# Kernel optimization log

Measured on AMD Instinct MI355X. Metric: run time of the kernel, lower is better.

Reference implementation:

```python
import jax, jax.numpy as jnp
import numpy as np

N = 100000   # amino-acid nodes
D = 128      # prot_hidden_dim == input_dim (output_dim)
E = 600000   # edges per relation
L = 3        # prot_num_layers
EPS = 1e-5   # BatchNorm eps


def setup_inputs() -> dict:
    key = jax.random.key(0)
    ks = jax.random.split(key, 16)
    x = jax.random.normal(ks[0], (N, D), jnp.float32)
    seq_src = jax.random.randint(ks[1], (E,), 0, N)
    seq_dst = jax.random.randint(ks[2], (E,), 0, N)
    knn_src = jax.random.randint(ks[3], (E,), 0, N)
    knn_dst = jax.random.randint(ks[4], (E,), 0, N)
    dis_src = jax.random.randint(ks[5], (E,), 0, N)
    dis_dst = jax.random.randint(ks[6], (E,), 0, N)
    # GraphConv weights/biases: [layer, relation, ...]
    Wrel = jax.random.normal(ks[7], (L, 3, D, D), jnp.float32) * (1.0 / np.sqrt(D))
    brel = jax.random.normal(ks[8], (L, 3, D), jnp.float32) * 0.02
    # per-layer fc (last maps hidden -> output_dim == D)
    Wfc = jax.random.normal(ks[9], (L, D, D), jnp.float32) * (1.0 / np.sqrt(D))
    bfc = jax.random.normal(ks[10], (L, D), jnp.float32) * 0.02
    # BatchNorm (eval mode) for layers l=0,1
    gamma = 1.0 + 0.1 * jax.random.normal(ks[11], (L - 1, D), jnp.float32)
    beta = 0.1 * jax.random.normal(ks[12], (L - 1, D), jnp.float32)
    run_mean = 0.1 * jax.random.normal(ks[13], (L - 1, D), jnp.float32)
    run_var = jax.random.uniform(ks[14], (L - 1, D), jnp.float32, 0.5, 1.5)
    return dict(x=x, seq_src=seq_src, seq_dst=seq_dst, knn_src=knn_src,
                knn_dst=knn_dst, dis_src=dis_src, dis_dst=dis_dst,
                Wrel=Wrel, brel=brel, Wfc=Wfc, bfc=bfc,
                gamma=gamma, beta=beta, run_mean=run_mean, run_var=run_var)


def _deg_norms(src, dst):
    # DGL norm='both': out-degree of src, in-degree of dst, clamped to >=1
    ones = jnp.ones(src.shape, jnp.float32)
    out_deg = jnp.clip(jax.ops.segment_sum(ones, src, num_segments=N), 1.0)
    in_deg = jnp.clip(jax.ops.segment_sum(ones, dst, num_segments=N), 1.0)
    return out_deg ** -0.5, in_deg ** -0.5


def reference(x, seq_src, seq_dst, knn_src, knn_dst, dis_src, dis_dst,
              Wrel, brel, Wfc, bfc, gamma, beta, run_mean, run_var):
    rels = [(seq_src, seq_dst), (knn_src, knn_dst), (dis_src, dis_dst)]
    norms = [_deg_norms(s, d) for s, d in rels]
    h = x
    for l in range(L):
        agg = jnp.zeros((N, D), h.dtype)
        for r, (s, d) in enumerate(rels):
            ns, nd = norms[r]
            # GraphConv norm='both', in==out feats: weight first, then propagate
            m = (h @ Wrel[l, r]) * ns[:, None]           # [N, D]
            msg = jax.ops.segment_sum(m[s], d, num_segments=N)  # gather-scatter
            agg = agg + msg * nd[:, None] + brel[l, r]
        h = agg @ Wfc[l] + bfc[l]
        if l < L - 1:
            # eval-mode BatchNorm1d + ReLU (dropout is identity in eval)
            h = (h - run_mean[l]) * jax.lax.rsqrt(run_var[l] + EPS) * gamma[l] + beta[l]
            h = jax.nn.relu(h)
    return h
```

## Files before the change

kernel.cpp:

```cpp
#include <hip/hip_runtime.h>
#include <math.h>

#define N_NODES 100000
#define D 128
#define E_EDGES 600000
#define BN_EPS 1e-5f

typedef __attribute__((ext_vector_type(8))) __bf16 bf16x8;
typedef __attribute__((ext_vector_type(4))) __bf16 bf16x4;
typedef __attribute__((ext_vector_type(16))) float f32x16;

__device__ __forceinline__ int qswz(int row, int q) {
    return (q & 8) | ((q ^ row) & 7);
}
__device__ __forceinline__ int swz(int row, int c) { return c ^ ((row >> 1) & 3); }

__global__ __launch_bounds__(256) void hist_kernel(
    const int* __restrict__ s0, const int* __restrict__ d0,
    const int* __restrict__ s1, const int* __restrict__ d1,
    const int* __restrict__ s2, const int* __restrict__ d2,
    int* __restrict__ outdeg, int* __restrict__ indeg)
{
    const int r = blockIdx.y;
    const int* src = (r == 0) ? s0 : ((r == 1) ? s1 : s2);
    const int* dst = (r == 0) ? d0 : ((r == 1) ? d1 : d2);
    int* od = outdeg + (size_t)r * N_NODES;
    int* id = indeg + (size_t)r * N_NODES;
    int i4 = blockIdx.x * 256 + threadIdx.x;
    if (i4 < E_EDGES / 4) {
        int4 s = ((const int4*)src)[i4];
        int4 d = ((const int4*)dst)[i4];
        atomicAdd(&od[s.x], 1); atomicAdd(&od[s.y], 1);
        atomicAdd(&od[s.z], 1); atomicAdd(&od[s.w], 1);
        atomicAdd(&id[d.x], 1); atomicAdd(&id[d.y], 1);
        atomicAdd(&id[d.z], 1); atomicAdd(&id[d.w], 1);
    }
}

__global__ __launch_bounds__(256) void norm_kernel(
    const int* __restrict__ outdeg, const int* __restrict__ indeg,
    float* __restrict__ ns, float* __restrict__ nd)
{
    int n = blockIdx.x * 256 + threadIdx.x;
    int r = blockIdx.y;
    if (n < N_NODES) {
        int od = outdeg[r * N_NODES + n];
        int id = indeg[r * N_NODES + n];
        ns[r * N_NODES + n] = rsqrtf((float)(od < 1 ? 1 : od));
        nd[r * N_NODES + n] = rsqrtf((float)(id < 1 ? 1 : id));
    }
}

__global__ __launch_bounds__(1024) void scan_kernel(
    const int* __restrict__ indeg, int* __restrict__ rowptr, int* __restrict__ cursor)
{
    const int r = blockIdx.x;
    const int4* deg4 = (const int4*)(indeg + (size_t)r * N_NODES);
    int* rp = rowptr + (size_t)r * (N_NODES + 1);
    int* cur = cursor + (size_t)r * N_NODES;

    __shared__ int wsum[16];
    __shared__ int woff[16];
    __shared__ int chunk_total;

    const int tid = threadIdx.x;
    const int lane = tid & 63;
    const int wid = tid >> 6;
    const int N4 = N_NODES / 4;

    int running = 0;
    for (int base4 = 0; base4 < N4; base4 += 1024) {
        int i4 = base4 + tid;
        int4 v = (i4 < N4) ? deg4[i4] : make_int4(0, 0, 0, 0);
        int s0 = v.x, s1 = s0 + v.y, s2 = s1 + v.z, s3 = s2 + v.w;

        int x = s3;
        #pragma unroll
        for (int off = 1; off < 64; off <<= 1) {
            int y = __shfl_up(x, off);
            if (lane >= off) x += y;
        }
        if (lane == 63) wsum[wid] = x;
        __syncthreads();
        if (wid == 0) {
            int t = (lane < 16) ? wsum[lane] : 0;
            int xx = t;
            #pragma unroll
            for (int off = 1; off < 16; off <<= 1) {
                int y = __shfl_up(xx, off);
                if (lane >= off) xx += y;
            }
            if (lane < 16) woff[lane] = xx - t;
            if (lane == 15) chunk_total = xx;
        }
        __syncthreads();

        int texcl = x - s3;
        int offset = running + woff[wid] + texcl;
        if (i4 < N4) {
            int idx = i4 * 4;
            rp[idx]     = offset;       cur[idx]     = offset;
            rp[idx + 1] = offset + s0;  cur[idx + 1] = offset + s0;
            rp[idx + 2] = offset + s1;  cur[idx + 2] = offset + s1;
            rp[idx + 3] = offset + s2;  cur[idx + 3] = offset + s2;
        }
        running += chunk_total;
    }
    if (tid == 0) rp[N_NODES] = running;
}

__global__ __launch_bounds__(256) void fill_kernel(
    const int* __restrict__ s0, const int* __restrict__ d0,
    const int* __restrict__ s1, const int* __restrict__ d1,
    const int* __restrict__ s2, const int* __restrict__ d2,
    const float* __restrict__ nsv,
    int* __restrict__ cursor, int2* __restrict__ eint)
{
    const int r = blockIdx.y;
    const int* src = (r == 0) ? s0 : ((r == 1) ? s1 : s2);
    const int* dst = (r == 0) ? d0 : ((r == 1) ? d1 : d2);
    int* cur = cursor + (size_t)r * N_NODES;
    int2* eg = eint + (size_t)r * E_EDGES;
    const float* ns_ = nsv + (size_t)r * N_NODES;
    int i = blockIdx.x * 256 + threadIdx.x;
    if (i < E_EDGES) {
        int s = src[i];
        int d = dst[i];
        int pos = atomicAdd(&cur[d], 1);
        eg[pos] = make_int2(s, __float_as_int(ns_[s]));
    }
}

__global__ __launch_bounds__(256) void wprep_kernel(
    const float* __restrict__ Wrel, const float* __restrict__ Wfc,
    const float* __restrict__ gma, const float* __restrict__ rvar,
    __bf16* __restrict__ Whi, __bf16* __restrict__ Wlo)
{
    __shared__ float W1[128][132];
    __shared__ float W2[128][132];
    const int b = blockIdx.x;
    const int l = b / 3;
    const int t = threadIdx.x;

    const float* src1 = Wrel + (size_t)b * D * D;
    const float* src2 = Wfc + (size_t)l * D * D;
    #pragma unroll
    for (int p = 0; p < 16; ++p) {
        int u = t + p * 256;
        int r = u >> 5, f = u & 31;
        float4 v1 = *(const float4*)(src1 + r * D + f * 4);
        float4 v2 = *(const float4*)(src2 + r * D + f * 4);
        *(float4*)&W1[r][f * 4] = v1;
        *(float4*)&W2[r][f * 4] = v2;
    }
    __syncthreads();

    const int row = t >> 1;
    const int cb = (t & 1) * 64;
    float4 acc4[16];
    #pragma unroll
    for (int j = 0; j < 16; ++j) acc4[j] = make_float4(0.f, 0.f, 0.f, 0.f);
    for (int k = 0; k < 128; ++k) {
        float a = W1[row][k];
        #pragma unroll
        for (int j = 0; j < 16; ++j) {
            float4 w = *(const float4*)&W2[k][cb + j * 4];
            acc4[j].x = fmaf(a, w.x, acc4[j].x);
            acc4[j].y = fmaf(a, w.y, acc4[j].y);
            acc4[j].z = fmaf(a, w.z, acc4[j].z);
            acc4[j].w = fmaf(a, w.w, acc4[j].w);
        }
    }
    for (int j = 0; j < 64; ++j) {
        int colj = cb + j;
        float s = 1.0f;
        if (l < 2) s = gma[l * D + colj] * rsqrtf(rvar[l * D + colj] + BN_EPS);
        float v = (&acc4[j >> 2].x)[j & 3] * s;
        __bf16 h = (__bf16)v;
        __bf16 lo = (__bf16)(v - (float)h);
        Whi[((size_t)b * D + colj) * D + row] = h;
        Wlo[((size_t)b * D + colj) * D + row] = lo;
    }
}

__global__ __launch_bounds__(128) void bias_prep_kernel(
    const float* __restrict__ brel, const float* __restrict__ Wfc,
    const float* __restrict__ bfc,
    const float* __restrict__ gma, const float* __restrict__ bta,
    const float* __restrict__ rmean, const float* __restrict__ rvar,
    float* __restrict__ bvec)
{
    int j = threadIdx.x;
    int l = blockIdx.x;
    float acc = bfc[l * D + j];
    for (int k = 0; k < D; ++k) {
        float bs = brel[(l * 3 + 0) * D + k] + brel[(l * 3 + 1) * D + k] + brel[(l * 3 + 2) * D + k];
        acc = fmaf(bs, Wfc[((size_t)l * D + k) * D + j], acc);
    }
    if (l < 2) {
        float s = gma[l * D + j] * rsqrtf(rvar[l * D + j] + BN_EPS);
        acc = acc * s + (bta[l * D + j] - rmean[l * D + j] * s);
    }
    bvec[l * D + j] = acc;
}

__global__ __launch_bounds__(512, 6) void fused_layer_kernel(
    const float* __restrict__ h,
    const int* __restrict__ rowptr,
    const int2* __restrict__ eint,
    const float* __restrict__ ndv,
    const __bf16* __restrict__ Whi,
    const __bf16* __restrict__ Wlo,
    float* __restrict__ out, const float* __restrict__ bias, int relu)
{
    __shared__ __bf16 Ah[64 * 128];
    __shared__ __bf16 Al[64 * 128];
    __shared__ __bf16 Bh[128 * 32];
    __shared__ __bf16 Bl[128 * 32];

    const int t = threadIdx.x;
    const int lane = t & 63;
    const int wid = t >> 6;
    const int wrow = wid & 1;
    const int wcol = wid >> 1;
    const int row0 = blockIdx.x * 64;

    const int g = t >> 3;
    const int gl = t & 7;

    f32x16 acc;
    #pragma unroll
    for (int i = 0; i < 16; ++i) acc[i] = 0.0f;

    for (int r = 0; r < 3; ++r) {
        const int* rp = rowptr + (size_t)r * (N_NODES + 1);
        const int2* eg = eint + (size_t)r * E_EDGES;
        const float* nd_ = ndv + (size_t)r * N_NODES;

        {
            int rowl = g;
            int grow = row0 + rowl;
            float4 a0 = {0,0,0,0}, a1 = {0,0,0,0}, a2 = {0,0,0,0}, a3 = {0,0,0,0};
            if (grow < N_NODES) {
                int beg = rp[grow], end = rp[grow + 1];
                float sc = nd_[grow];
                int e = beg;
                for (; e + 1 < end; e += 2) {
                    int2 e0 = eg[e];
                    int2 e1 = eg[e + 1];
                    float w0 = __int_as_float(e0.y);
                    float w1 = __int_as_float(e1.y);
                    const float* hp0 = h + (size_t)e0.x * D + gl * 4;
                    const float* hp1 = h + (size_t)e1.x * D + gl * 4;
                    float4 u0 = *(const float4*)(hp0);
                    float4 u1 = *(const float4*)(hp0 + 32);
                    float4 u2 = *(const float4*)(hp0 + 64);
                    float4 u3 = *(const float4*)(hp0 + 96);
                    float4 v0 = *(const float4*)(hp1);
                    float4 v1 = *(const float4*)(hp1 + 32);
                    float4 v2 = *(const float4*)(hp1 + 64);
                    float4 v3 = *(const float4*)(hp1 + 96);
                    a0.x = fmaf(w0, u0.x, a0.x); a0.y = fmaf(w0, u0.y, a0.y);
                    a0.z = fmaf(w0, u0.z, a0.z); a0.w = fmaf(w0, u0.w, a0.w);
                    a1.x = fmaf(w0, u1.x, a1.x); a1.y = fmaf(w0, u1.y, a1.y);
                    a1.z = fmaf(w0, u1.z, a1.z); a1.w = fmaf(w0, u1.w, a1.w);
                    a2.x = fmaf(w0, u2.x, a2.x); a2.y = fmaf(w0, u2.y, a2.y);
                    a2.z = fmaf(w0, u2.z, a2.z); a2.w = fmaf(w0, u2.w, a2.w);
                    a3.x = fmaf(w0, u3.x, a3.x); a3.y = fmaf(w0, u3.y, a3.y);
                    a3.z = fmaf(w0, u3.z, a3.z); a3.w = fmaf(w0, u3.w, a3.w);
                    a0.x = fmaf(w1, v0.x, a0.x); a0.y = fmaf(w1, v0.y, a0.y);
                    a0.z = fmaf(w1, v0.z, a0.z); a0.w = fmaf(w1, v0.w, a0.w);
                    a1.x = fmaf(w1, v1.x, a1.x); a1.y = fmaf(w1, v1.y, a1.y);
                    a1.z = fmaf(w1, v1.z, a1.z); a1.w = fmaf(w1, v1.w, a1.w);
                    a2.x = fmaf(w1, v2.x, a2.x); a2.y = fmaf(w1, v2.y, a2.y);
                    a2.z = fmaf(w1, v2.z, a2.z); a2.w = fmaf(w1, v2.w, a2.w);
                    a3.x = fmaf(w1, v3.x, a3.x); a3.y = fmaf(w1, v3.y, a3.y);
                    a3.z = fmaf(w1, v3.z, a3.z); a3.w = fmaf(w1, v3.w, a3.w);
                }
                if (e < end) {
                    int2 e0 = eg[e];
                    float w0 = __int_as_float(e0.y);
                    const float* hp0 = h + (size_t)e0.x * D + gl * 4;
                    float4 u0 = *(const float4*)(hp0);
                    float4 u1 = *(const float4*)(hp0 + 32);
                    float4 u2 = *(const float4*)(hp0 + 64);
                    float4 u3 = *(const float4*)(hp0 + 96);
                    a0.x = fmaf(w0, u0.x, a0.x); a0.y = fmaf(w0, u0.y, a0.y);
                    a0.z = fmaf(w0, u0.z, a0.z); a0.w = fmaf(w0, u0.w, a0.w);
                    a1.x = fmaf(w0, u1.x, a1.x); a1.y = fmaf(w0, u1.y, a1.y);
                    a1.z = fmaf(w0, u1.z, a1.z); a1.w = fmaf(w0, u1.w, a1.w);
                    a2.x = fmaf(w0, u2.x, a2.x); a2.y = fmaf(w0, u2.y, a2.y);
                    a2.z = fmaf(w0, u2.z, a2.z); a2.w = fmaf(w0, u2.w, a2.w);
                    a3.x = fmaf(w0, u3.x, a3.x); a3.y = fmaf(w0, u3.y, a3.y);
                    a3.z = fmaf(w0, u3.z, a3.z); a3.w = fmaf(w0, u3.w, a3.w);
                }
                a0.x *= sc; a0.y *= sc; a0.z *= sc; a0.w *= sc;
                a1.x *= sc; a1.y *= sc; a1.z *= sc; a1.w *= sc;
                a2.x *= sc; a2.y *= sc; a2.z *= sc; a2.w *= sc;
                a3.x *= sc; a3.y *= sc; a3.z *= sc; a3.w *= sc;
            }
            float4 av[4] = {a0, a1, a2, a3};
            #pragma unroll
            for (int j = 0; j < 4; ++j) {
                int q = (gl >> 1) + 4 * j;
                int idx = rowl * 128 + qswz(rowl, q) * 8 + (gl & 1) * 4;
                bf16x4 hv, lv;
                float* ap = &av[j].x;
                #pragma unroll
                for (int c = 0; c < 4; ++c) {
                    __bf16 hb = (__bf16)ap[c];
                    hv[c] = hb;
                    lv[c] = (__bf16)(ap[c] - (float)hb);
                }
                *(bf16x4*)&Ah[idx] = hv;
                *(bf16x4*)&Al[idx] = lv;
            }
        }

        for (int ks = 0; ks < 4; ++ks) {
            {
                int colj = t >> 2;
                int c = t & 3;
                int idx = colj * 32 + swz(colj, c) * 8;
                const __bf16* sh = Whi + (size_t)r * D * D + (size_t)colj * D + ks * 32 + c * 8;
                const __bf16* sl = Wlo + (size_t)r * D * D + (size_t)colj * D + ks * 32 + c * 8;
                *(bf16x8*)&Bh[idx] = *(const bf16x8*)sh;
                *(bf16x8*)&Bl[idx] = *(const bf16x8*)sl;
            }
            __syncthreads();

            const int arow = lane & 31;
            const int kgrp = lane >> 5;
            #pragma unroll
            for (int ksub = 0; ksub < 2; ++ksub) {
                int ac = ksub * 2 + kgrp;
                int arow_g = wrow * 32 + arow;
                int q = ks * 4 + ac;
                int aidx = arow_g * 128 + qswz(arow_g, q) * 8;
                bf16x8 ahv = *(const bf16x8*)&Ah[aidx];
                bf16x8 alv = *(const bf16x8*)&Al[aidx];
                int colg = wcol * 32 + arow;
                int bidx = colg * 32 + swz(colg, ac) * 8;
                bf16x8 bhv = *(const bf16x8*)&Bh[bidx];
                bf16x8 blv = *(const bf16x8*)&Bl[bidx];
                acc = __builtin_amdgcn_mfma_f32_32x32x16_bf16(ahv, bhv, acc, 0, 0, 0);
                acc = __builtin_amdgcn_mfma_f32_32x32x16_bf16(ahv, blv, acc, 0, 0, 0);
                acc = __builtin_amdgcn_mfma_f32_32x32x16_bf16(alv, bhv, acc, 0, 0, 0);
            }
            __syncthreads();
        }
    }

    const int colb = lane & 31;
    const int rq = lane >> 5;
    {
        int colg = wcol * 32 + colb;
        float bv = bias[colg];
        #pragma unroll
        for (int reg = 0; reg < 16; ++reg) {
            int rowl = wrow * 32 + (reg & 3) + 8 * (reg >> 2) + 4 * rq;
            int grow = row0 + rowl;
            if (grow < N_NODES) {
                float z = acc[reg] + bv;
                if (relu) z = z > 0.f ? z : 0.f;
                out[(size_t)grow * D + colg] = z;
            }
        }
    }
}

extern "C" void kernel_launch(void* const* d_in, const int* in_sizes, int n_in,
                              void* d_out, int out_size, void* d_ws, size_t ws_size,
                              hipStream_t stream)
{
    const float* x      = (const float*)d_in[0];
    const int* seq_src  = (const int*)d_in[1];
    const int* seq_dst  = (const int*)d_in[2];
    const int* knn_src  = (const int*)d_in[3];
    const int* knn_dst  = (const int*)d_in[4];
    const int* dis_src  = (const int*)d_in[5];
    const int* dis_dst  = (const int*)d_in[6];
    const float* Wrel   = (const float*)d_in[7];
    const float* brel   = (const float*)d_in[8];
    const float* Wfc    = (const float*)d_in[9];
    const float* bfc    = (const float*)d_in[10];
    const float* gma    = (const float*)d_in[11];
    const float* bta    = (const float*)d_in[12];
    const float* rmean  = (const float*)d_in[13];
    const float* rvar   = (const float*)d_in[14];
    float* out = (float*)d_out;

    const size_t ND = (size_t)N_NODES * D;
    float* ws   = (float*)d_ws;
    float* h0   = ws;
    float* h1   = h0 + ND;
    float* ns_  = h1 + ND;
    float* nd_  = ns_ + 3 * N_NODES;
    float* bvec = nd_ + 3 * N_NODES;
    __bf16* Whi = (__bf16*)(bvec + 3 * D);
    __bf16* Wlo = Whi + (size_t)9 * D * D;
    int* outdeg = (int*)(Wlo + (size_t)9 * D * D);
    int* indeg  = outdeg + 3 * N_NODES;
    int* rowptr = indeg + 3 * N_NODES;
    int* cursor = rowptr + 3 * (N_NODES + 1) + 1;
    int2* eint  = (int2*)(cursor + 3 * N_NODES);

    hipMemsetAsync(outdeg, 0, (size_t)6 * N_NODES * sizeof(int), stream);
    hist_kernel<<<dim3((E_EDGES / 4 + 255) / 256, 3), 256, 0, stream>>>(
        seq_src, seq_dst, knn_src, knn_dst, dis_src, dis_dst, outdeg, indeg);
    norm_kernel<<<dim3((N_NODES + 255) / 256, 3), 256, 0, stream>>>(outdeg, indeg, ns_, nd_);
    scan_kernel<<<3, 1024, 0, stream>>>(indeg, rowptr, cursor);
    fill_kernel<<<dim3((E_EDGES + 255) / 256, 3), 256, 0, stream>>>(
        seq_src, seq_dst, knn_src, knn_dst, dis_src, dis_dst, ns_, cursor, eint);

    wprep_kernel<<<9, 256, 0, stream>>>(Wrel, Wfc, gma, rvar, Whi, Wlo);
    bias_prep_kernel<<<3, 128, 0, stream>>>(brel, Wfc, bfc, gma, bta, rmean, rvar, bvec);

    const int GB = (N_NODES + 63) / 64;
    fused_layer_kernel<<<GB, 512, 0, stream>>>(
        x, rowptr, eint, nd_, Whi, Wlo, h0, bvec, 1);
    fused_layer_kernel<<<GB, 512, 0, stream>>>(
        h0, rowptr, eint, nd_, Whi + (size_t)3 * D * D, Wlo + (size_t)3 * D * D,
        h1, bvec + D, 1);
    fused_layer_kernel<<<GB, 512, 0, stream>>>(
        h1, rowptr, eint, nd_, Whi + (size_t)6 * D * D, Wlo + (size_t)6 * D * D,
        out, bvec + 2 * D, 0);
}
```

Before: 946.0 us.

## Parallelize CSR scan and enlarge fused layer tiles to 128 rows

Replaces the three-block serial prefix scan with a three-kernel decoupled scan (per-block partial, mid carry, add), so building the CSR row pointers uses many blocks. The fused gather+MFMA layer kernel moves to 128-row tiles with 1024 threads: each 16-lane group gathers two rows with contiguous 8-float segments and 4-way edge unrolling, the LDS swizzle is simplified, and B staging is issued right after each k-step barrier instead of before it. Output stores become nontemporal. The larger block raises LDS use and register pressure and halves the number of blocks, which may reduce occupancy or load balance.

```diff
diff --git a/kernel.cpp b/kernel.cpp
--- a/kernel.cpp
+++ b/kernel.cpp
@@ -5,14 +5,15 @@
 #define D 128
 #define E_EDGES 600000
 #define BN_EPS 1e-5f
+#define RPS (N_NODES + 4)
+#define N4V (N_NODES / 4)
+#define SCAN_BLOCKS ((N4V + 255) / 256)
 
 typedef __attribute__((ext_vector_type(8))) __bf16 bf16x8;
 typedef __attribute__((ext_vector_type(4))) __bf16 bf16x4;
 typedef __attribute__((ext_vector_type(16))) float f32x16;
 
-__device__ __forceinline__ int qswz(int row, int q) {
-    return (q & 8) | ((q ^ row) & 7);
-}
+__device__ __forceinline__ int qswz(int row, int q) { return q ^ (row & 15); }
 __device__ __forceinline__ int swz(int row, int c) { return c ^ ((row >> 1) & 3); }
 
 __global__ __launch_bounds__(256) void hist_kernel(
@@ -51,62 +52,72 @@
     }
 }
 
-__global__ __launch_bounds__(1024) void scan_kernel(
-    const int* __restrict__ indeg, int* __restrict__ rowptr, int* __restrict__ cursor)
-{
-    const int r = blockIdx.x;
-    const int4* deg4 = (const int4*)(indeg + (size_t)r * N_NODES);
-    int* rp = rowptr + (size_t)r * (N_NODES + 1);
-    int* cur = cursor + (size_t)r * N_NODES;
-
-    __shared__ int wsum[16];
-    __shared__ int woff[16];
-    __shared__ int chunk_total;
-
-    const int tid = threadIdx.x;
-    const int lane = tid & 63;
-    const int wid = tid >> 6;
-    const int N4 = N_NODES / 4;
-
-    int running = 0;
-    for (int base4 = 0; base4 < N4; base4 += 1024) {
-        int i4 = base4 + tid;
-        int4 v = (i4 < N4) ? deg4[i4] : make_int4(0, 0, 0, 0);
-        int s0 = v.x, s1 = s0 + v.y, s2 = s1 + v.z, s3 = s2 + v.w;
-
-        int x = s3;
+__global__ __launch_bounds__(256) void scan_part_kernel(
+    const int* __restrict__ indeg, int* __restrict__ rowptr, int* __restrict__ bsum)
+{
+    const int r = blockIdx.y;
+    const int t = threadIdx.x;
+    const int lane = t & 63, wid = t >> 6;
+    __shared__ int wsum[4], woff[4];
+    int i4 = blockIdx.x * 256 + t;
+    int4 v = (i4 < N4V) ? ((const int4*)(indeg + (size_t)r * N_NODES))[i4]
+                        : make_int4(0, 0, 0, 0);
+    int s0 = v.x, s1 = s0 + v.y, s2 = s1 + v.z, s3 = s2 + v.w;
+    int x = s3;
+    #pragma unroll
+    for (int off = 1; off < 64; off <<= 1) {
+        int y = __shfl_up(x, off);
+        if (lane >= off) x += y;
+    }
+    if (lane == 63) wsum[wid] = x;
+    __syncthreads();
+    if (t < 4) { int s = 0; for (int j = 0; j < t; ++j) s += wsum[j]; woff[t] = s; }
+    __syncthreads();
+    int base = woff[wid] + (x - s3);
+    if (i4 < N4V) {
+        int idx = i4 * 4;
+        int* rp = rowptr + (size_t)r * RPS;
+        rp[idx] = base; rp[idx + 1] = base + s0; rp[idx + 2] = base + s1; rp[idx + 3] = base + s2;
+    }
+    if (t == 255) bsum[r * SCAN_BLOCKS + blockIdx.x] = woff[3] + wsum[3];
+}
+
+__global__ __launch_bounds__(256) void scan_mid_kernel(
+    int* __restrict__ bsum, int* __restrict__ rowptr)
+{
+    const int t = threadIdx.x;
+    const int lane = t & 63, wid = t >> 6;
+    if (wid >= 3) return;
+    const int r = wid;
+    int carry = 0;
+    for (int c = 0; c < (SCAN_BLOCKS + 63) / 64; ++c) {
+        int idx = c * 64 + lane;
+        int v = (idx < SCAN_BLOCKS) ? bsum[r * SCAN_BLOCKS + idx] : 0;
+        int x = v;
         #pragma unroll
         for (int off = 1; off < 64; off <<= 1) {
             int y = __shfl_up(x, off);
             if (lane >= off) x += y;
         }
-        if (lane == 63) wsum[wid] = x;
-        __syncthreads();
-        if (wid == 0) {
-            int t = (lane < 16) ? wsum[lane] : 0;
-            int xx = t;
-            #pragma unroll
-            for (int off = 1; off < 16; off <<= 1) {
-                int y = __shfl_up(xx, off);
-                if (lane >= off) xx += y;
-            }
-            if (lane < 16) woff[lane] = xx - t;
-            if (lane == 15) chunk_total = xx;
-        }
-        __syncthreads();
-
-        int texcl = x - s3;
-        int offset = running + woff[wid] + texcl;
-        if (i4 < N4) {
-            int idx = i4 * 4;
-            rp[idx]     = offset;       cur[idx]     = offset;
-            rp[idx + 1] = offset + s0;  cur[idx + 1] = offset + s0;
-            rp[idx + 2] = offset + s1;  cur[idx + 2] = offset + s1;
-            rp[idx + 3] = offset + s2;  cur[idx + 3] = offset + s2;
-        }
-        running += chunk_total;
-    }
-    if (tid == 0) rp[N_NODES] = running;
+        if (idx < SCAN_BLOCKS) bsum[r * SCAN_BLOCKS + idx] = carry + x - v;
+        carry += __shfl(x, 63);
+    }
+    if (lane == 0) rowptr[(size_t)r * RPS + N_NODES] = carry;
+}
+
+__global__ __launch_bounds__(256) void scan_add_kernel(
+    int* __restrict__ rowptr, const int* __restrict__ bsum, int* __restrict__ cursor)
+{
+    const int r = blockIdx.y;
+    int i4 = blockIdx.x * 256 + threadIdx.x;
+    if (i4 < N4V) {
+        int off = bsum[r * SCAN_BLOCKS + blockIdx.x];
+        int4* rp4 = (int4*)(rowptr + (size_t)r * RPS);
+        int4 v = rp4[i4];
+        v.x += off; v.y += off; v.z += off; v.w += off;
+        rp4[i4] = v;
+        ((int4*)(cursor + (size_t)r * N_NODES))[i4] = v;
+    }
 }
 
 __global__ __launch_bounds__(256) void fill_kernel(
@@ -204,7 +215,13 @@
     bvec[l * D + j] = acc;
 }
 
-__global__ __launch_bounds__(512, 6) void fused_layer_kernel(
+#define FMA8(W_, U_, V_)                                                       \
+    acc0.x = fmaf(W_, U_.x, acc0.x); acc0.y = fmaf(W_, U_.y, acc0.y);          \
+    acc0.z = fmaf(W_, U_.z, acc0.z); acc0.w = fmaf(W_, U_.w, acc0.w);          \
+    acc1.x = fmaf(W_, V_.x, acc1.x); acc1.y = fmaf(W_, V_.y, acc1.y);          \
+    acc1.z = fmaf(W_, V_.z, acc1.z); acc1.w = fmaf(W_, V_.w, acc1.w);
+
+__global__ __launch_bounds__(1024, 8) void fused_layer_kernel(
     const float* __restrict__ h,
     const int* __restrict__ rowptr,
     const int2* __restrict__ eint,
@@ -213,130 +230,107 @@
     const __bf16* __restrict__ Wlo,
     float* __restrict__ out, const float* __restrict__ bias, int relu)
 {
-    __shared__ __bf16 Ah[64 * 128];
-    __shared__ __bf16 Al[64 * 128];
+    __shared__ __bf16 Ah[128 * 128];
+    __shared__ __bf16 Al[128 * 128];
     __shared__ __bf16 Bh[128 * 32];
     __shared__ __bf16 Bl[128 * 32];
 
     const int t = threadIdx.x;
     const int lane = t & 63;
     const int wid = t >> 6;
-    const int wrow = wid & 1;
-    const int wcol = wid >> 1;
-    const int row0 = blockIdx.x * 64;
-
-    const int g = t >> 3;
-    const int gl = t & 7;
+    const int wrow = wid & 3;
+    const int wcol = wid >> 2;
+    const int row0 = blockIdx.x * 128;
+    const int g = t >> 4;
+    const int gl = t & 15;
 
     f32x16 acc;
     #pragma unroll
     for (int i = 0; i < 16; ++i) acc[i] = 0.0f;
 
+    auto stageB = [&](int r_, int ks_) {
+        int half = t & 1;
+        int u = t >> 1;
+        int colj = u >> 2;
+        int c = u & 3;
+        const __bf16* srcp = (half ? Wlo : Whi) + (size_t)r_ * D * D + (size_t)colj * D + ks_ * 32 + c * 8;
+        __bf16* dstp = (half ? Bl : Bh) + colj * 32 + swz(colj, c) * 8;
+        *(bf16x8*)dstp = *(const bf16x8*)srcp;
+    };
+
     for (int r = 0; r < 3; ++r) {
-        const int* rp = rowptr + (size_t)r * (N_NODES + 1);
+        const int* rp = rowptr + (size_t)r * RPS;
         const int2* eg = eint + (size_t)r * E_EDGES;
         const float* nd_ = ndv + (size_t)r * N_NODES;
 
-        {
-            int rowl = g;
+        stageB(r, 0);
+
+        #pragma unroll
+        for (int rr = 0; rr < 2; ++rr) {
+            int rowl = g * 2 + rr;
             int grow = row0 + rowl;
-            float4 a0 = {0,0,0,0}, a1 = {0,0,0,0}, a2 = {0,0,0,0}, a3 = {0,0,0,0};
+            float4 acc0 = {0, 0, 0, 0}, acc1 = {0, 0, 0, 0};
             if (grow < N_NODES) {
                 int beg = rp[grow], end = rp[grow + 1];
                 float sc = nd_[grow];
                 int e = beg;
-                for (; e + 1 < end; e += 2) {
-                    int2 e0 = eg[e];
-                    int2 e1 = eg[e + 1];
-                    float w0 = __int_as_float(e0.y);
-                    float w1 = __int_as_float(e1.y);
-                    const float* hp0 = h + (size_t)e0.x * D + gl * 4;
-                    const float* hp1 = h + (size_t)e1.x * D + gl * 4;
-                    float4 u0 = *(const float4*)(hp0);
-                    float4 u1 = *(const float4*)(hp0 + 32);
-                    float4 u2 = *(const float4*)(hp0 + 64);
-                    float4 u3 = *(const float4*)(hp0 + 96);
-                    float4 v0 = *(const float4*)(hp1);
-                    float4 v1 = *(const float4*)(hp1 + 32);
-                    float4 v2 = *(const float4*)(hp1 + 64);
-                    float4 v3 = *(const float4*)(hp1 + 96);
-                    a0.x = fmaf(w0, u0.x, a0.x); a0.y = fmaf(w0, u0.y, a0.y);
-                    a0.z = fmaf(w0, u0.z, a0.z); a0.w = fmaf(w0, u0.w, a0.w);
-                    a1.x = fmaf(w0, u1.x, a1.x); a1.y = fmaf(w0, u1.y, a1.y);
-                    a1.z = fmaf(w0, u1.z, a1.z); a1.w = fmaf(w0, u1.w, a1.w);
-                    a2.x = fmaf(w0, u2.x, a2.x); a2.y = fmaf(w0, u2.y, a2.y);
-                    a2.z = fmaf(w0, u2.z, a2.z); a2.w = fmaf(w0, u2.w, a2.w);
-                    a3.x = fmaf(w0, u3.x, a3.x); a3.y = fmaf(w0, u3.y, a3.y);
-                    a3.z = fmaf(w0, u3.z, a3.z); a3.w = fmaf(w0, u3.w, a3.w);
-                    a0.x = fmaf(w1, v0.x, a0.x); a0.y = fmaf(w1, v0.y, a0.y);
-                    a0.z = fmaf(w1, v0.z, a0.z); a0.w = fmaf(w1, v0.w, a0.w);
-                    a1.x = fmaf(w1, v1.x, a1.x); a1.y = fmaf(w1, v1.y, a1.y);
-                    a1.z = fmaf(w1, v1.z, a1.z); a1.w = fmaf(w1, v1.w, a1.w);
-                    a2.x = fmaf(w1, v2.x, a2.x); a2.y = fmaf(w1, v2.y, a2.y);
-                    a2.z = fmaf(w1, v2.z, a2.z); a2.w = fmaf(w1, v2.w, a2.w);
-                    a3.x = fmaf(w1, v3.x, a3.x); a3.y = fmaf(w1, v3.y, a3.y);
-                    a3.z = fmaf(w1, v3.z, a3.z); a3.w = fmaf(w1, v3.w, a3.w);
+                for (; e + 4 <= end; e += 4) {
+                    int2 r0 = eg[e], r1 = eg[e + 1], r2 = eg[e + 2], r3 = eg[e + 3];
+                    const float* p0 = h + (size_t)r0.x * D + gl * 8;
+                    const float* p1 = h + (size_t)r1.x * D + gl * 8;
+                    const float* p2 = h + (size_t)r2.x * D + gl * 8;
+                    const float* p3 = h + (size_t)r3.x * D + gl * 8;
+                    float4 u0 = *(const float4*)p0, v0 = *(const float4*)(p0 + 4);
+                    float4 u1 = *(const float4*)p1, v1 = *(const float4*)(p1 + 4);
+                    float4 u2 = *(const float4*)p2, v2 = *(const float4*)(p2 + 4);
+                    float4 u3 = *(const float4*)p3, v3 = *(const float4*)(p3 + 4);
+                    float w0 = __int_as_float(r0.y), w1 = __int_as_float(r1.y);
+                    float w2 = __int_as_float(r2.y), w3 = __int_as_float(r3.y);
+                    FMA8(w0, u0, v0); FMA8(w1, u1, v1);
+                    FMA8(w2, u2, v2); FMA8(w3, u3, v3);
+                }
+                if (e + 2 <= end) {
+                    int2 r0 = eg[e], r1 = eg[e + 1];
+                    const float* p0 = h + (size_t)r0.x * D + gl * 8;
+                    const float* p1 = h + (size_t)r1.x * D + gl * 8;
+                    float4 u0 = *(const float4*)p0, v0 = *(const float4*)(p0 + 4);
+                    float4 u1 = *(const float4*)p1, v1 = *(const float4*)(p1 + 4);
+                    float w0 = __int_as_float(r0.y), w1 = __int_as_float(r1.y);
+                    FMA8(w0, u0, v0); FMA8(w1, u1, v1);
+                    e += 2;
                 }
                 if (e < end) {
-                    int2 e0 = eg[e];
-                    float w0 = __int_as_float(e0.y);
-                    const float* hp0 = h + (size_t)e0.x * D + gl * 4;
-                    float4 u0 = *(const float4*)(hp0);
-                    float4 u1 = *(const float4*)(hp0 + 32);
-                    float4 u2 = *(const float4*)(hp0 + 64);
-                    float4 u3 = *(const float4*)(hp0 + 96);
-                    a0.x = fmaf(w0, u0.x, a0.x); a0.y = fmaf(w0, u0.y, a0.y);
-                    a0.z = fmaf(w0, u0.z, a0.z); a0.w = fmaf(w0, u0.w, a0.w);
-                    a1.x = fmaf(w0, u1.x, a1.x); a1.y = fmaf(w0, u1.y, a1.y);
-                    a1.z = fmaf(w0, u1.z, a1.z); a1.w = fmaf(w0, u1.w, a1.w);
-                    a2.x = fmaf(w0, u2.x, a2.x); a2.y = fmaf(w0, u2.y, a2.y);
-                    a2.z = fmaf(w0, u2.z, a2.z); a2.w = fmaf(w0, u2.w, a2.w);
-                    a3.x = fmaf(w0, u3.x, a3.x); a3.y = fmaf(w0, u3.y, a3.y);
-                    a3.z = fmaf(w0, u3.z, a3.z); a3.w = fmaf(w0, u3.w, a3.w);
+                    int2 r0 = eg[e];
+                    const float* p0 = h + (size_t)r0.x * D + gl * 8;
+                    float4 u0 = *(const float4*)p0, v0 = *(const float4*)(p0 + 4);
+                    float w0 = __int_as_float(r0.y);
+                    FMA8(w0, u0, v0);
                 }
-                a0.x *= sc; a0.y *= sc; a0.z *= sc; a0.w *= sc;
-                a1.x *= sc; a1.y *= sc; a1.z *= sc; a1.w *= sc;
-                a2.x *= sc; a2.y *= sc; a2.z *= sc; a2.w *= sc;
-                a3.x *= sc; a3.y *= sc; a3.z *= sc; a3.w *= sc;
+                acc0.x *= sc; acc0.y *= sc; acc0.z *= sc; acc0.w *= sc;
+                acc1.x *= sc; acc1.y *= sc; acc1.z *= sc; acc1.w *= sc;
             }
-            float4 av[4] = {a0, a1, a2, a3};
+            float a[8] = {acc0.x, acc0.y, acc0.z, acc0.w, acc1.x, acc1.y, acc1.z, acc1.w};
+            bf16x8 hv, lv;
             #pragma unroll
-            for (int j = 0; j < 4; ++j) {
-                int q = (gl >> 1) + 4 * j;
-                int idx = rowl * 128 + qswz(rowl, q) * 8 + (gl & 1) * 4;
-                bf16x4 hv, lv;
-                float* ap = &av[j].x;
-                #pragma unroll
-                for (int c = 0; c < 4; ++c) {
-                    __bf16 hb = (__bf16)ap[c];
-                    hv[c] = hb;
-                    lv[c] = (__bf16)(ap[c] - (float)hb);
-                }
-                *(bf16x4*)&Ah[idx] = hv;
-                *(bf16x4*)&Al[idx] = lv;
+            for (int c = 0; c < 8; ++c) {
+                __bf16 hb = (__bf16)a[c];
+                hv[c] = hb;
+                lv[c] = (__bf16)(a[c] - (float)hb);
             }
+            int idxA = rowl * 128 + qswz(rowl, gl) * 8;
+            *(bf16x8*)&Ah[idxA] = hv;
+            *(bf16x8*)&Al[idxA] = lv;
         }
 
         for (int ks = 0; ks < 4; ++ks) {
-            {
-                int colj = t >> 2;
-                int c = t & 3;
-                int idx = colj * 32 + swz(colj, c) * 8;
-                const __bf16* sh = Whi + (size_t)r * D * D + (size_t)colj * D + ks * 32 + c * 8;
-                const __bf16* sl = Wlo + (size_t)r * D * D + (size_t)colj * D + ks * 32 + c * 8;
-                *(bf16x8*)&Bh[idx] = *(const bf16x8*)sh;
-                *(bf16x8*)&Bl[idx] = *(const bf16x8*)sl;
-            }
             __syncthreads();
-
             const int arow = lane & 31;
             const int kgrp = lane >> 5;
             #pragma unroll
             for (int ksub = 0; ksub < 2; ++ksub) {
                 int ac = ksub * 2 + kgrp;
                 int arow_g = wrow * 32 + arow;
-                int q = ks * 4 + ac;
-                int aidx = arow_g * 128 + qswz(arow_g, q) * 8;
+                int aidx = arow_g * 128 + qswz(arow_g, ks * 4 + ac) * 8;
                 bf16x8 ahv = *(const bf16x8*)&Ah[aidx];
                 bf16x8 alv = *(const bf16x8*)&Al[aidx];
                 int colg = wcol * 32 + arow;
@@ -348,6 +342,7 @@
                 acc = __builtin_amdgcn_mfma_f32_32x32x16_bf16(alv, bhv, acc, 0, 0, 0);
             }
             __syncthreads();
+            if (ks < 3) stageB(r, ks + 1);
         }
     }
 
@@ -362,8 +357,8 @@
             int grow = row0 + rowl;
             if (grow < N_NODES) {
                 float z = acc[reg] + bv;
-                if (relu) z = z > 0.f ? z : 0.f;
-                out[(size_t)grow * D + colg] = z;
+                if (relu) z = fmaxf(z, 0.f);
+                __builtin_nontemporal_store(z, &out[(size_t)grow * D + colg]);
             }
         }
     }
@@ -402,27 +397,30 @@
     int* outdeg = (int*)(Wlo + (size_t)9 * D * D);
     int* indeg  = outdeg + 3 * N_NODES;
     int* rowptr = indeg + 3 * N_NODES;
-    int* cursor = rowptr + 3 * (N_NODES + 1) + 1;
-    int2* eint  = (int2*)(cursor + 3 * N_NODES);
+    int* cursor = rowptr + 3 * RPS;
+    int* bsum   = cursor + 3 * N_NODES;
+    int2* eint  = (int2*)(bsum + 3 * SCAN_BLOCKS + 2);
 
     hipMemsetAsync(outdeg, 0, (size_t)6 * N_NODES * sizeof(int), stream);
     hist_kernel<<<dim3((E_EDGES / 4 + 255) / 256, 3), 256, 0, stream>>>(
         seq_src, seq_dst, knn_src, knn_dst, dis_src, dis_dst, outdeg, indeg);
     norm_kernel<<<dim3((N_NODES + 255) / 256, 3), 256, 0, stream>>>(outdeg, indeg, ns_, nd_);
-    scan_kernel<<<3, 1024, 0, stream>>>(indeg, rowptr, cursor);
+    scan_part_kernel<<<dim3(SCAN_BLOCKS, 3), 256, 0, stream>>>(indeg, rowptr, bsum);
+    scan_mid_kernel<<<1, 256, 0, stream>>>(bsum, rowptr);
+    scan_add_kernel<<<dim3(SCAN_BLOCKS, 3), 256, 0, stream>>>(rowptr, bsum, cursor);
     fill_kernel<<<dim3((E_EDGES + 255) / 256, 3), 256, 0, stream>>>(
         seq_src, seq_dst, knn_src, knn_dst, dis_src, dis_dst, ns_, cursor, eint);
 
     wprep_kernel<<<9, 256, 0, stream>>>(Wrel, Wfc, gma, rvar, Whi, Wlo);
     bias_prep_kernel<<<3, 128, 0, stream>>>(brel, Wfc, bfc, gma, bta, rmean, rvar, bvec);
 
-    const int GB = (N_NODES + 63) / 64;
-    fused_layer_kernel<<<GB, 512, 0, stream>>>(
+    const int GB = (N_NODES + 127) / 128;
+    fused_layer_kernel<<<GB, 1024, 0, stream>>>(
         x, rowptr, eint, nd_, Whi, Wlo, h0, bvec, 1);
-    fused_layer_kernel<<<GB, 512, 0, stream>>>(
+    fused_layer_kernel<<<GB, 1024, 0, stream>>>(
         h0, rowptr, eint, nd_, Whi + (size_t)3 * D * D, Wlo + (size_t)3 * D * D,
         h1, bvec + D, 1);
-    fused_layer_kernel<<<GB, 512, 0, stream>>>(
+    fused_layer_kernel<<<GB, 1024, 0, stream>>>(
         h1, rowptr, eint, nd_, Whi + (size_t)6 * D * D, Wlo + (size_t)6 * D * D,
         out, bvec + 2 * D, 0);
 }
```

Measured after the change: 1.103 ms. +16.6%, slower.
